# Optimization experiments

Measured on AMD Instinct MI355X. Metric: run time of the kernel, lower is better.

Reference implementation:

```python
import jax, jax.numpy as jnp
import numpy as np

B, N, C, G = 32, 1024, 64, 64

def setup_inputs() -> dict:
    key = jax.random.key(0)
    ks = jax.random.split(key, 8)
    return {
        "x": jax.random.normal(ks[0], (B, N, C), dtype=jnp.float32),
        "valid_len": jax.random.randint(ks[1], (B,), 0, N, dtype=jnp.int64) if jax.config.jax_enable_x64 else jax.random.randint(ks[1], (B,), 0, N, dtype=jnp.int32),
        "Wq": jax.random.normal(ks[2], (C, G), dtype=jnp.float32) * 0.1,
        "bq": jax.random.normal(ks[3], (G,), dtype=jnp.float32) * 0.1,
        "Wk": jax.random.normal(ks[4], (C, G), dtype=jnp.float32) * 0.1,
        "bk": jax.random.normal(ks[5], (G,), dtype=jnp.float32) * 0.1,
        "Wv": jax.random.normal(ks[6], (C, G), dtype=jnp.float32) * 0.1,
        "bv": jax.random.normal(ks[7], (G,), dtype=jnp.float32) * 0.1,
    }

def reference(x, valid_len, Wq, bq, Wk, bk, Wv, bv):
    # x: [B, N, C]; valid_len: [B] int (number of valid key positions per batch)
    q = x @ Wq + bq                                   # [B, N, G]
    k = x @ Wk + bk                                   # [B, N, G]
    v = x @ Wv + bv                                   # [B, N, G]
    scores = jnp.einsum('bnd,bmd->bnm', q, k)         # [B, N, N] (no 1/sqrt(d) scale)
    # mask: key positions >= valid_len[b] get -1e6 (matches original's -1000000.0 fill)
    col = jnp.arange(scores.shape[-1])
    mask = col[None, None, :] >= valid_len[:, None, None]
    scores = jnp.where(mask, jnp.float32(-1000000.0), scores)
    attn = jax.nn.softmax(scores, axis=-1)            # [B, N, N]
    return jnp.einsum('bnm,bmd->bnd', attn, v)        # [B, N, G]
```

## Files before the change

### kernel.cpp

```cpp
#include <hip/hip_runtime.h>
#include <stdint.h>


typedef __attribute__((ext_vector_type(4))) float    floatx4;
typedef __attribute__((ext_vector_type(8))) _Float16 halfx8;

static __device__ __forceinline__ unsigned short f2h(float f) {
    union { _Float16 h; unsigned short u; } v; v.h = (_Float16)f;
    return v.u;
}
static __device__ __forceinline__ float h2f(unsigned short u) {
    union { unsigned short u; _Float16 h; } v; v.u = u;
    return (float)v.h;
}

__global__ __launch_bounds__(256) void qkv_proj_kernel(
    const float* __restrict__ x,
    const float* __restrict__ Wq, const float* __restrict__ bq,
    const float* __restrict__ Wk, const float* __restrict__ bk,
    const float* __restrict__ Wv, const float* __restrict__ bv,
    unsigned short* __restrict__ q_ws, unsigned short* __restrict__ k_ws,
    unsigned short* __restrict__ vt_ws)
{
    __shared__ __align__(16) unsigned short smem[8 * 64 * 64];
    float* vtmp = (float*)&smem[2 * 64 * 64];

    const int XS_HI = 0, XS_LO = 64 * 64;
    #define WT_OFF(i) (2 * 64 * 64 + (i) * 64 * 64)

    const int tid  = threadIdx.x;
    const int blk  = blockIdx.x;
    const int row0 = blk * 64;
    const int b    = blk >> 4;
    const int n0   = (blk & 15) * 64;
    const int lane = tid & 63;
    const int w    = tid >> 6;
    const int l15  = lane & 15;
    const int quad = lane >> 4;

#pragma unroll
    for (int i = 0; i < 2; ++i) {
        int id = i * 256 + tid;
        int r = id >> 3, c8 = id & 7;
        const float4* gp = (const float4*)(x + (row0 + r) * 64 + c8 * 8);
        float4 f0 = gp[0], f1 = gp[1];
        float fv[8] = { f0.x, f0.y, f0.z, f0.w, f1.x, f1.y, f1.z, f1.w };
        __align__(16) unsigned short thi[8], tlo[8];
#pragma unroll
        for (int j = 0; j < 8; ++j) {
            unsigned short hi = f2h(fv[j]);
            thi[j] = hi;
            tlo[j] = f2h(fv[j] - h2f(hi));
        }
        int idx = r * 64 + ((c8 ^ (r & 7)) * 8);
        *(uint4*)&smem[XS_HI + idx] = *(uint4*)thi;
        *(uint4*)&smem[XS_LO + idx] = *(uint4*)tlo;
    }
    {
        const float* Ws[3] = { Wq, Wk, Wv };
        int g = tid & 63, ci = tid >> 6;
#pragma unroll
        for (int wi = 0; wi < 3; ++wi) {
#pragma unroll
            for (int j = 0; j < 16; ++j) {
                int c = ci * 16 + j;
                float f = Ws[wi][c * 64 + g];
                unsigned short hi = f2h(f);
                unsigned short lo = f2h(f - h2f(hi));
                int c8 = c >> 3;
                int idx = g * 64 + ((c8 ^ (g & 7)) * 8) + (c & 7);
                smem[WT_OFF(wi * 2 + 0) + idx] = hi;
                smem[WT_OFF(wi * 2 + 1) + idx] = lo;
            }
        }
    }
    __syncthreads();

    const int arow = w * 16 + l15;
    const int aidx0 = arow * 64 + (((0 + quad) ^ (arow & 7)) * 8);
    const int aidx1 = arow * 64 + (((4 + quad) ^ (arow & 7)) * 8);
    halfx8 a_hi0 = *(const halfx8*)&smem[XS_HI + aidx0];
    halfx8 a_hi1 = *(const halfx8*)&smem[XS_HI + aidx1];
    halfx8 a_lo0 = *(const halfx8*)&smem[XS_LO + aidx0];
    halfx8 a_lo1 = *(const halfx8*)&smem[XS_LO + aidx1];

    const float* biases[3] = { bq, bk, bv };
    floatx4 vacc[4];
#pragma unroll
    for (int wi = 0; wi < 3; ++wi) {
#pragma unroll
        for (int gs = 0; gs < 4; ++gs) {
            int g0 = gs * 16;
            float bias = biases[wi][g0 + l15];
            floatx4 acc = { bias, bias, bias, bias };
            int brow = g0 + l15;
            int bidx0 = brow * 64 + (((0 + quad) ^ (brow & 7)) * 8);
            int bidx1 = brow * 64 + (((4 + quad) ^ (brow & 7)) * 8);
            halfx8 b_hi0 = *(const halfx8*)&smem[WT_OFF(wi * 2 + 0) + bidx0];
            halfx8 b_hi1 = *(const halfx8*)&smem[WT_OFF(wi * 2 + 0) + bidx1];
            halfx8 b_lo0 = *(const halfx8*)&smem[WT_OFF(wi * 2 + 1) + bidx0];
            halfx8 b_lo1 = *(const halfx8*)&smem[WT_OFF(wi * 2 + 1) + bidx1];
            acc = __builtin_amdgcn_mfma_f32_16x16x32_f16(a_hi0, b_hi0, acc, 0, 0, 0);
            acc = __builtin_amdgcn_mfma_f32_16x16x32_f16(a_hi1, b_hi1, acc, 0, 0, 0);
            acc = __builtin_amdgcn_mfma_f32_16x16x32_f16(a_hi0, b_lo0, acc, 0, 0, 0);
            acc = __builtin_amdgcn_mfma_f32_16x16x32_f16(a_hi1, b_lo1, acc, 0, 0, 0);
            acc = __builtin_amdgcn_mfma_f32_16x16x32_f16(a_lo0, b_hi0, acc, 0, 0, 0);
            acc = __builtin_amdgcn_mfma_f32_16x16x32_f16(a_lo1, b_hi1, acc, 0, 0, 0);
            if (wi < 2) {
                unsigned short* dst = (wi == 0) ? q_ws : k_ws;
#pragma unroll
                for (int r = 0; r < 4; ++r) {
                    int row = row0 + w * 16 + quad * 4 + r;
                    dst[row * 64 + g0 + l15] = f2h(acc[r]);
                }
            } else {
                vacc[gs] = acc;
            }
        }
    }

    __syncthreads();
#pragma unroll
    for (int gs = 0; gs < 4; ++gs) {
#pragma unroll
        for (int r = 0; r < 4; ++r) {
            int nl = w * 16 + quad * 4 + r;
            vtmp[(gs * 16 + l15) * 65 + nl] = vacc[gs][r];
        }
    }
    __syncthreads();

    {
        int g = tid >> 2, c4 = tid & 3;
        __align__(16) unsigned short tmp[16];
#pragma unroll
        for (int j = 0; j < 16; ++j) tmp[j] = f2h(vtmp[g * 65 + c4 * 16 + j]);
        unsigned short* dst = vt_ws + (b * 64 + g) * 1024 + n0 + c4 * 16;
        *(uint4*)(dst)     = ((uint4*)tmp)[0];
        *(uint4*)(dst + 8) = ((uint4*)tmp)[1];
    }
    #undef WT_OFF
}

__global__ __launch_bounds__(256) void attn_kernel(
    const unsigned short* __restrict__ q_ws, const unsigned short* __restrict__ k_ws,
    const unsigned short* __restrict__ vt_ws, const int* __restrict__ valid_len,
    float* __restrict__ out)
{
    __shared__ __align__(16) unsigned short qs[64 * 64];
    __shared__ __align__(16) unsigned short ks[64 * 64];
    __shared__ __align__(16) unsigned short vs[64 * 64];
    __shared__ __align__(16) float ps[4][16 * 68];

    const int tid  = threadIdx.x;
    const int blk  = blockIdx.x;
    const int b    = blk >> 4;
    const int row0 = blk * 64;
    const int lane = tid & 63;
    const int w    = tid >> 6;
    const int l15  = lane & 15;
    const int quad = lane >> 4;

#pragma unroll
    for (int i = 0; i < 2; ++i) {
        int id = i * 256 + tid;
        int r = id >> 3, c8 = id & 7;
        uint4 d = *(const uint4*)(q_ws + (row0 + r) * 64 + c8 * 8);
        *(uint4*)&qs[r * 64 + ((c8 ^ (r & 7)) * 8)] = d;
    }

    const int vl = valid_len[b];
    const int ntiles = (vl == 0) ? 16 : ((vl + 63) >> 6);

    float m_r[4] = { -INFINITY, -INFINITY, -INFINITY, -INFINITY };
    float l_r[4] = { 0.f, 0.f, 0.f, 0.f };
    floatx4 o[4] = { {0,0,0,0}, {0,0,0,0}, {0,0,0,0}, {0,0,0,0} };

    const int arow = w * 16 + l15;

    for (int t = 0; t < ntiles; ++t) {
        __syncthreads();
#pragma unroll
        for (int i = 0; i < 2; ++i) {
            int id = i * 256 + tid;
            int r = id >> 3, c8 = id & 7;
            uint4 dk = *(const uint4*)(k_ws + (b * 1024 + t * 64 + r) * 64 + c8 * 8);
            *(uint4*)&ks[r * 64 + ((c8 ^ (r & 7)) * 8)] = dk;
            uint4 dv = *(const uint4*)(vt_ws + (b * 64 + r) * 1024 + t * 64 + c8 * 8);
            *(uint4*)&vs[r * 64 + ((c8 ^ (r & 7)) * 8)] = dv;
        }
        __syncthreads();

        halfx8 aq0 = *(const halfx8*)&qs[arow * 64 + (((0 + quad) ^ (arow & 7)) * 8)];
        halfx8 aq1 = *(const halfx8*)&qs[arow * 64 + (((4 + quad) ^ (arow & 7)) * 8)];

        floatx4 s[4];
#pragma unroll
        for (int sub = 0; sub < 4; ++sub) {
            int krow = sub * 16 + l15;
            halfx8 bk0 = *(const halfx8*)&ks[krow * 64 + (((0 + quad) ^ (krow & 7)) * 8)];
            halfx8 bk1 = *(const halfx8*)&ks[krow * 64 + (((4 + quad) ^ (krow & 7)) * 8)];
            floatx4 acc = { 0, 0, 0, 0 };
            acc = __builtin_amdgcn_mfma_f32_16x16x32_f16(aq0, bk0, acc, 0, 0, 0);
            acc = __builtin_amdgcn_mfma_f32_16x16x32_f16(aq1, bk1, acc, 0, 0, 0);
            int key = t * 64 + sub * 16 + l15;
            if (key >= vl) { acc[0] = -1e6f; acc[1] = -1e6f; acc[2] = -1e6f; acc[3] = -1e6f; }
            s[sub] = acc;
        }

        float p[4][4];
        float alpha[4];
#pragma unroll
        for (int r = 0; r < 4; ++r) {
            float mx = fmaxf(fmaxf(s[0][r], s[1][r]), fmaxf(s[2][r], s[3][r]));
#pragma unroll
            for (int off = 1; off < 16; off <<= 1)
                mx = fmaxf(mx, __shfl_xor(mx, off, 64));
            float mnew = fmaxf(m_r[r], mx);
            alpha[r] = __expf(m_r[r] - mnew);
            float sum = 0.f;
#pragma unroll
            for (int sub = 0; sub < 4; ++sub) {
                float pv = __expf(s[sub][r] - mnew);
                p[sub][r] = pv;
                sum += pv;
            }
#pragma unroll
            for (int off = 1; off < 16; off <<= 1)
                sum += __shfl_xor(sum, off, 64);
            l_r[r] = l_r[r] * alpha[r] + sum;
            m_r[r] = mnew;
        }
#pragma unroll
        for (int gs = 0; gs < 4; ++gs) {
            o[gs][0] *= alpha[0]; o[gs][1] *= alpha[1];
            o[gs][2] *= alpha[2]; o[gs][3] *= alpha[3];
        }

        float* psw = ps[w];
#pragma unroll
        for (int sub = 0; sub < 4; ++sub)
#pragma unroll
            for (int r = 0; r < 4; ++r)
                psw[(quad * 4 + r) * 68 + sub * 16 + l15] = p[sub][r];

        halfx8 ap[2];
#pragma unroll
        for (int kc = 0; kc < 2; ++kc) {
            const float* src = &psw[l15 * 68 + kc * 32 + quad * 8];
            float4 f0 = *(const float4*)src;
            float4 f1 = *(const float4*)(src + 4);
            __align__(16) unsigned short tmp[8] = {
                f2h(f0.x), f2h(f0.y), f2h(f0.z), f2h(f0.w),
                f2h(f1.x), f2h(f1.y), f2h(f1.z), f2h(f1.w) };
            ap[kc] = *(halfx8*)tmp;
        }

#pragma unroll
        for (int gs = 0; gs < 4; ++gs) {
            int grow = gs * 16 + l15;
            halfx8 bv0 = *(const halfx8*)&vs[grow * 64 + (((0 + quad) ^ (grow & 7)) * 8)];
            halfx8 bv1 = *(const halfx8*)&vs[grow * 64 + (((4 + quad) ^ (grow & 7)) * 8)];
            o[gs] = __builtin_amdgcn_mfma_f32_16x16x32_f16(ap[0], bv0, o[gs], 0, 0, 0);
            o[gs] = __builtin_amdgcn_mfma_f32_16x16x32_f16(ap[1], bv1, o[gs], 0, 0, 0);
        }
    }

#pragma unroll
    for (int gs = 0; gs < 4; ++gs) {
#pragma unroll
        for (int r = 0; r < 4; ++r) {
            int row = row0 + w * 16 + quad * 4 + r;
            out[row * 64 + gs * 16 + l15] = o[gs][r] / l_r[r];
        }
    }
}

extern "C" void kernel_launch(void* const* d_in, const int* in_sizes, int n_in,
                              void* d_out, int out_size, void* d_ws, size_t ws_size,
                              hipStream_t stream) {
    const float* x    = (const float*)d_in[0];
    const int*   vlen = (const int*)  d_in[1];
    const float* Wq   = (const float*)d_in[2];
    const float* bq   = (const float*)d_in[3];
    const float* Wk   = (const float*)d_in[4];
    const float* bk   = (const float*)d_in[5];
    const float* Wv   = (const float*)d_in[6];
    const float* bv   = (const float*)d_in[7];
    float* out = (float*)d_out;

    unsigned short* q_ws  = (unsigned short*)d_ws;
    unsigned short* k_ws  = q_ws + 32768 * 64;
    unsigned short* vt_ws = k_ws + 32768 * 64;

    qkv_proj_kernel<<<512, 256, 0, stream>>>(x, Wq, bq, Wk, bk, Wv, bv, q_ws, k_ws, vt_ws);
    attn_kernel<<<512, 256, 0, stream>>>(q_ws, k_ws, vt_ws, vlen, out);
}
```

Before: 108.5 us.

## Use two-pass softmax with exact row max, double-buffered K/V tiles and half P staging

The attention kernel now makes a first pass over K tiles to find the exact row max, then a second pass computing exp, row sums and P·V with no online rescaling or per-tile shuffle reductions. K/V tiles are double-buffered in LDS with register prefetch, and masking runs only on partial tiles. P is staged in LDS as swizzled half instead of float. The projection kernel writes Q/K through LDS for coalesced 16-byte global stores. The trade-off is that QK^T is computed twice and K is loaded twice.

```diff
diff --git a/kernel.cpp b/kernel.cpp
--- a/kernel.cpp
+++ b/kernel.cpp
@@ -22,11 +22,11 @@
     unsigned short* __restrict__ q_ws, unsigned short* __restrict__ k_ws,
     unsigned short* __restrict__ vt_ws)
 {
-    __shared__ __align__(16) unsigned short smem[8 * 64 * 64];
-    float* vtmp = (float*)&smem[2 * 64 * 64];
-
-    const int XS_HI = 0, XS_LO = 64 * 64;
-    #define WT_OFF(i) (2 * 64 * 64 + (i) * 64 * 64)
+    __shared__ __align__(16) unsigned short smem[8 * 4096];
+    float* vtmp = (float*)&smem[2 * 4096];
+
+    const int XS_HI = 0, XS_LO = 4096;
+    #define WT_OFF(i) (2 * 4096 + (i) * 4096)
 
     const int tid  = threadIdx.x;
     const int blk  = blockIdx.x;
@@ -83,6 +83,11 @@
     halfx8 a_hi1 = *(const halfx8*)&smem[XS_HI + aidx1];
     halfx8 a_lo0 = *(const halfx8*)&smem[XS_LO + aidx0];
     halfx8 a_lo1 = *(const halfx8*)&smem[XS_LO + aidx1];
+
+    __syncthreads();
+
+    unsigned short* q_lds = &smem[0];
+    unsigned short* k_lds = &smem[4096];
 
     const float* biases[3] = { bq, bk, bv };
     floatx4 vacc[4];
@@ -107,11 +112,12 @@
             acc = __builtin_amdgcn_mfma_f32_16x16x32_f16(a_lo0, b_hi0, acc, 0, 0, 0);
             acc = __builtin_amdgcn_mfma_f32_16x16x32_f16(a_lo1, b_hi1, acc, 0, 0, 0);
             if (wi < 2) {
-                unsigned short* dst = (wi == 0) ? q_ws : k_ws;
+                unsigned short* dst = (wi == 0) ? q_lds : k_lds;
+                int c8 = gs * 2 + (l15 >> 3);
 #pragma unroll
                 for (int r = 0; r < 4; ++r) {
-                    int row = row0 + w * 16 + quad * 4 + r;
-                    dst[row * 64 + g0 + l15] = f2h(acc[r]);
+                    int row = w * 16 + quad * 4 + r;
+                    dst[row * 64 + ((c8 ^ (row & 7)) * 8) + (l15 & 7)] = f2h(acc[r]);
                 }
             } else {
                 vacc[gs] = acc;
@@ -120,6 +126,16 @@
     }
 
     __syncthreads();
+
+#pragma unroll
+    for (int i = 0; i < 2; ++i) {
+        int id = i * 256 + tid;
+        int r = id >> 3, c8 = id & 7;
+        int sidx = r * 64 + ((c8 ^ (r & 7)) * 8);
+        *(uint4*)(q_ws + (row0 + r) * 64 + c8 * 8) = *(const uint4*)&q_lds[sidx];
+        *(uint4*)(k_ws + (row0 + r) * 64 + c8 * 8) = *(const uint4*)&k_lds[sidx];
+    }
+
 #pragma unroll
     for (int gs = 0; gs < 4; ++gs) {
 #pragma unroll
@@ -129,7 +145,6 @@
         }
     }
     __syncthreads();
-
     {
         int g = tid >> 2, c4 = tid & 3;
         __align__(16) unsigned short tmp[16];
@@ -147,10 +162,10 @@
     const unsigned short* __restrict__ vt_ws, const int* __restrict__ valid_len,
     float* __restrict__ out)
 {
-    __shared__ __align__(16) unsigned short qs[64 * 64];
-    __shared__ __align__(16) unsigned short ks[64 * 64];
-    __shared__ __align__(16) unsigned short vs[64 * 64];
-    __shared__ __align__(16) float ps[4][16 * 68];
+    __shared__ __align__(16) unsigned short qs[4096];
+    __shared__ __align__(16) unsigned short kbuf[2][4096];
+    __shared__ __align__(16) unsigned short vbuf[2][4096];
+    __shared__ __align__(16) unsigned short ps[4 * 1024];
 
     const int tid  = threadIdx.x;
     const int blk  = blockIdx.x;
@@ -161,117 +176,174 @@
     const int l15  = lane & 15;
     const int quad = lane >> 4;
 
-#pragma unroll
-    for (int i = 0; i < 2; ++i) {
-        int id = i * 256 + tid;
-        int r = id >> 3, c8 = id & 7;
-        uint4 d = *(const uint4*)(q_ws + (row0 + r) * 64 + c8 * 8);
-        *(uint4*)&qs[r * 64 + ((c8 ^ (r & 7)) * 8)] = d;
-    }
-
-    const int vl = valid_len[b];
-    const int ntiles = (vl == 0) ? 16 : ((vl + 63) >> 6);
-
-    float m_r[4] = { -INFINITY, -INFINITY, -INFINITY, -INFINITY };
-    float l_r[4] = { 0.f, 0.f, 0.f, 0.f };
-    floatx4 o[4] = { {0,0,0,0}, {0,0,0,0}, {0,0,0,0}, {0,0,0,0} };
+    const int r_a  = tid >> 3,          c8_a = tid & 7;
+    const int r_b  = (256 + tid) >> 3,  c8_b = tid & 7;
+    const int lidx_a = r_a * 64 + ((c8_a ^ (r_a & 7)) * 8);
+    const int lidx_b = r_b * 64 + ((c8_b ^ (r_b & 7)) * 8);
+
+    *(uint4*)&qs[lidx_a] = *(const uint4*)(q_ws + (row0 + r_a) * 64 + c8_a * 8);
+    *(uint4*)&qs[lidx_b] = *(const uint4*)(q_ws + (row0 + r_b) * 64 + c8_b * 8);
+
+    const int vl    = valid_len[b];
+    const float mv  = (vl > 0) ? -1000000.0f : 0.0f;
+    const int nt    = (vl == 0) ? 16 : ((vl + 63) >> 6);
+    const int fullt = vl >> 6;
+
+    const unsigned short* kbase = k_ws + (size_t)b * 1024 * 64;
+    const unsigned short* vbase = vt_ws + (size_t)b * 64 * 1024;
+
+    uint4 kr0 = *(const uint4*)(kbase + r_a * 64 + c8_a * 8);
+    uint4 kr1 = *(const uint4*)(kbase + r_b * 64 + c8_b * 8);
+    *(uint4*)&kbuf[0][lidx_a] = kr0;
+    *(uint4*)&kbuf[0][lidx_b] = kr1;
+
+    __syncthreads();
 
     const int arow = w * 16 + l15;
-
-    for (int t = 0; t < ntiles; ++t) {
+    halfx8 aq0 = *(const halfx8*)&qs[arow * 64 + (((0 + quad) ^ (arow & 7)) * 8)];
+    halfx8 aq1 = *(const halfx8*)&qs[arow * 64 + (((4 + quad) ^ (arow & 7)) * 8)];
+
+    float m_lane[4] = { -1000000.0f, -1000000.0f, -1000000.0f, -1000000.0f };
+    for (int t = 0; t < nt; ++t) {
+        bool pre = (t + 1) < nt;
+        if (pre) {
+            const unsigned short* kp = kbase + (t + 1) * 64 * 64;
+            kr0 = *(const uint4*)(kp + r_a * 64 + c8_a * 8);
+            kr1 = *(const uint4*)(kp + r_b * 64 + c8_b * 8);
+        }
         __syncthreads();
-#pragma unroll
-        for (int i = 0; i < 2; ++i) {
-            int id = i * 256 + tid;
-            int r = id >> 3, c8 = id & 7;
-            uint4 dk = *(const uint4*)(k_ws + (b * 1024 + t * 64 + r) * 64 + c8 * 8);
-            *(uint4*)&ks[r * 64 + ((c8 ^ (r & 7)) * 8)] = dk;
-            uint4 dv = *(const uint4*)(vt_ws + (b * 64 + r) * 1024 + t * 64 + c8 * 8);
-            *(uint4*)&vs[r * 64 + ((c8 ^ (r & 7)) * 8)] = dv;
-        }
-        __syncthreads();
-
-        halfx8 aq0 = *(const halfx8*)&qs[arow * 64 + (((0 + quad) ^ (arow & 7)) * 8)];
-        halfx8 aq1 = *(const halfx8*)&qs[arow * 64 + (((4 + quad) ^ (arow & 7)) * 8)];
+        if (pre) {
+            *(uint4*)&kbuf[(t + 1) & 1][lidx_a] = kr0;
+            *(uint4*)&kbuf[(t + 1) & 1][lidx_b] = kr1;
+        }
+        const unsigned short* ksb = kbuf[t & 1];
 
         floatx4 s[4];
 #pragma unroll
         for (int sub = 0; sub < 4; ++sub) {
             int krow = sub * 16 + l15;
-            halfx8 bk0 = *(const halfx8*)&ks[krow * 64 + (((0 + quad) ^ (krow & 7)) * 8)];
-            halfx8 bk1 = *(const halfx8*)&ks[krow * 64 + (((4 + quad) ^ (krow & 7)) * 8)];
+            halfx8 bk0 = *(const halfx8*)&ksb[krow * 64 + (((0 + quad) ^ (krow & 7)) * 8)];
+            halfx8 bk1 = *(const halfx8*)&ksb[krow * 64 + (((4 + quad) ^ (krow & 7)) * 8)];
             floatx4 acc = { 0, 0, 0, 0 };
             acc = __builtin_amdgcn_mfma_f32_16x16x32_f16(aq0, bk0, acc, 0, 0, 0);
             acc = __builtin_amdgcn_mfma_f32_16x16x32_f16(aq1, bk1, acc, 0, 0, 0);
-            int key = t * 64 + sub * 16 + l15;
-            if (key >= vl) { acc[0] = -1e6f; acc[1] = -1e6f; acc[2] = -1e6f; acc[3] = -1e6f; }
             s[sub] = acc;
         }
-
-        float p[4][4];
-        float alpha[4];
-#pragma unroll
-        for (int r = 0; r < 4; ++r) {
-            float mx = fmaxf(fmaxf(s[0][r], s[1][r]), fmaxf(s[2][r], s[3][r]));
-#pragma unroll
-            for (int off = 1; off < 16; off <<= 1)
-                mx = fmaxf(mx, __shfl_xor(mx, off, 64));
-            float mnew = fmaxf(m_r[r], mx);
-            alpha[r] = __expf(m_r[r] - mnew);
-            float sum = 0.f;
+        if (t >= fullt) {
 #pragma unroll
             for (int sub = 0; sub < 4; ++sub) {
-                float pv = __expf(s[sub][r] - mnew);
-                p[sub][r] = pv;
-                sum += pv;
-            }
-#pragma unroll
-            for (int off = 1; off < 16; off <<= 1)
-                sum += __shfl_xor(sum, off, 64);
-            l_r[r] = l_r[r] * alpha[r] + sum;
-            m_r[r] = mnew;
-        }
-#pragma unroll
-        for (int gs = 0; gs < 4; ++gs) {
-            o[gs][0] *= alpha[0]; o[gs][1] *= alpha[1];
-            o[gs][2] *= alpha[2]; o[gs][3] *= alpha[3];
-        }
-
-        float* psw = ps[w];
-#pragma unroll
-        for (int sub = 0; sub < 4; ++sub)
-#pragma unroll
-            for (int r = 0; r < 4; ++r)
-                psw[(quad * 4 + r) * 68 + sub * 16 + l15] = p[sub][r];
-
-        halfx8 ap[2];
-#pragma unroll
-        for (int kc = 0; kc < 2; ++kc) {
-            const float* src = &psw[l15 * 68 + kc * 32 + quad * 8];
-            float4 f0 = *(const float4*)src;
-            float4 f1 = *(const float4*)(src + 4);
-            __align__(16) unsigned short tmp[8] = {
-                f2h(f0.x), f2h(f0.y), f2h(f0.z), f2h(f0.w),
-                f2h(f1.x), f2h(f1.y), f2h(f1.z), f2h(f1.w) };
-            ap[kc] = *(halfx8*)tmp;
-        }
+                int key = t * 64 + sub * 16 + l15;
+                if (key >= vl) { s[sub][0] = mv; s[sub][1] = mv; s[sub][2] = mv; s[sub][3] = mv; }
+            }
+        }
+#pragma unroll
+        for (int r = 0; r < 4; ++r)
+            m_lane[r] = fmaxf(m_lane[r],
+                        fmaxf(fmaxf(s[0][r], s[1][r]), fmaxf(s[2][r], s[3][r])));
+    }
+
+    float m[4];
+#pragma unroll
+    for (int r = 0; r < 4; ++r) {
+        float mm = m_lane[r];
+#pragma unroll
+        for (int off = 1; off < 16; off <<= 1)
+            mm = fmaxf(mm, __shfl_xor(mm, off, 64));
+        m[r] = mm;
+    }
+
+    kr0 = *(const uint4*)(kbase + r_a * 64 + c8_a * 8);
+    kr1 = *(const uint4*)(kbase + r_b * 64 + c8_b * 8);
+    uint4 vr0 = *(const uint4*)(vbase + r_a * 1024 + c8_a * 8);
+    uint4 vr1 = *(const uint4*)(vbase + r_b * 1024 + c8_b * 8);
+    __syncthreads();
+    *(uint4*)&kbuf[0][lidx_a] = kr0;
+    *(uint4*)&kbuf[0][lidx_b] = kr1;
+    *(uint4*)&vbuf[0][lidx_a] = vr0;
+    *(uint4*)&vbuf[0][lidx_b] = vr1;
+
+    float l_lane[4] = { 0.f, 0.f, 0.f, 0.f };
+    floatx4 o[4] = { {0,0,0,0}, {0,0,0,0}, {0,0,0,0}, {0,0,0,0} };
+
+    for (int t = 0; t < nt; ++t) {
+        bool pre = (t + 1) < nt;
+        if (pre) {
+            const unsigned short* kp = kbase + (t + 1) * 64 * 64;
+            const unsigned short* vp = vbase + (t + 1) * 64;
+            kr0 = *(const uint4*)(kp + r_a * 64 + c8_a * 8);
+            kr1 = *(const uint4*)(kp + r_b * 64 + c8_b * 8);
+            vr0 = *(const uint4*)(vp + r_a * 1024 + c8_a * 8);
+            vr1 = *(const uint4*)(vp + r_b * 1024 + c8_b * 8);
+        }
+        __syncthreads();
+        if (pre) {
+            *(uint4*)&kbuf[(t + 1) & 1][lidx_a] = kr0;
+            *(uint4*)&kbuf[(t + 1) & 1][lidx_b] = kr1;
+            *(uint4*)&vbuf[(t + 1) & 1][lidx_a] = vr0;
+            *(uint4*)&vbuf[(t + 1) & 1][lidx_b] = vr1;
+        }
+        const unsigned short* ksb = kbuf[t & 1];
+        const unsigned short* vsb = vbuf[t & 1];
+
+        floatx4 s[4];
+#pragma unroll
+        for (int sub = 0; sub < 4; ++sub) {
+            int krow = sub * 16 + l15;
+            halfx8 bk0 = *(const halfx8*)&ksb[krow * 64 + (((0 + quad) ^ (krow & 7)) * 8)];
+            halfx8 bk1 = *(const halfx8*)&ksb[krow * 64 + (((4 + quad) ^ (krow & 7)) * 8)];
+            floatx4 acc = { 0, 0, 0, 0 };
+            acc = __builtin_amdgcn_mfma_f32_16x16x32_f16(aq0, bk0, acc, 0, 0, 0);
+            acc = __builtin_amdgcn_mfma_f32_16x16x32_f16(aq1, bk1, acc, 0, 0, 0);
+            s[sub] = acc;
+        }
+        if (t >= fullt) {
+#pragma unroll
+            for (int sub = 0; sub < 4; ++sub) {
+                int key = t * 64 + sub * 16 + l15;
+                if (key >= vl) { s[sub][0] = mv; s[sub][1] = mv; s[sub][2] = mv; s[sub][3] = mv; }
+            }
+        }
+
+        unsigned short* psw = &ps[w * 1024];
+#pragma unroll
+        for (int sub = 0; sub < 4; ++sub) {
+            int c8 = sub * 2 + (l15 >> 3);
+#pragma unroll
+            for (int r = 0; r < 4; ++r) {
+                float p = __expf(s[sub][r] - m[r]);
+                l_lane[r] += p;
+                int row = quad * 4 + r;
+                psw[row * 64 + ((c8 ^ (row & 7)) * 8) + (l15 & 7)] = f2h(p);
+            }
+        }
+        halfx8 ap0 = *(const halfx8*)&psw[l15 * 64 + (((0 + quad) ^ (l15 & 7)) * 8)];
+        halfx8 ap1 = *(const halfx8*)&psw[l15 * 64 + (((4 + quad) ^ (l15 & 7)) * 8)];
 
 #pragma unroll
         for (int gs = 0; gs < 4; ++gs) {
             int grow = gs * 16 + l15;
-            halfx8 bv0 = *(const halfx8*)&vs[grow * 64 + (((0 + quad) ^ (grow & 7)) * 8)];
-            halfx8 bv1 = *(const halfx8*)&vs[grow * 64 + (((4 + quad) ^ (grow & 7)) * 8)];
-            o[gs] = __builtin_amdgcn_mfma_f32_16x16x32_f16(ap[0], bv0, o[gs], 0, 0, 0);
-            o[gs] = __builtin_amdgcn_mfma_f32_16x16x32_f16(ap[1], bv1, o[gs], 0, 0, 0);
-        }
-    }
-
+            halfx8 bv0 = *(const halfx8*)&vsb[grow * 64 + (((0 + quad) ^ (grow & 7)) * 8)];
+            halfx8 bv1 = *(const halfx8*)&vsb[grow * 64 + (((4 + quad) ^ (grow & 7)) * 8)];
+            o[gs] = __builtin_amdgcn_mfma_f32_16x16x32_f16(ap0, bv0, o[gs], 0, 0, 0);
+            o[gs] = __builtin_amdgcn_mfma_f32_16x16x32_f16(ap1, bv1, o[gs], 0, 0, 0);
+        }
+    }
+
+    float l[4];
+#pragma unroll
+    for (int r = 0; r < 4; ++r) {
+        float ss = l_lane[r];
+#pragma unroll
+        for (int off = 1; off < 16; off <<= 1)
+            ss += __shfl_xor(ss, off, 64);
+        l[r] = ss;
+    }
 #pragma unroll
     for (int gs = 0; gs < 4; ++gs) {
 #pragma unroll
         for (int r = 0; r < 4; ++r) {
             int row = row0 + w * 16 + quad * 4 + r;
-            out[row * 64 + gs * 16 + l15] = o[gs][r] / l_r[r];
+            out[row * 64 + gs * 16 + l15] = o[gs][r] / l[r];
         }
     }
 }
```

Measured after the change: 106.8 us. About the same (-1.5%).
